# Kernel tuning notes

Hardware: AMD Instinct MI355X
Metric: run time of the kernel (lower is better)

The kernel has to match this reference:

```python
import jax, jax.numpy as jnp
import numpy as np

K_F = 3
NUM = K_F * K_F - 1      # 8 non-reference neighbors
IDX_REF = NUM // 2       # 4: reference pixel inserted in the middle
PROP_TIME = 18


def _conv2d(x, w, b, pad):
    y = jax.lax.conv_general_dilated(x, w, (1, 1), [(pad, pad), (pad, pad)],
                                     dimension_numbers=("NCHW", "OIHW", "NCHW"))
    return y + b[None, :, None, None]


def _offset_affinity(guidance, conv_w, conv_b, aff_scale):
    # TGASS branch of _get_offset_affinity
    B, _, H, W = guidance.shape
    pad_g = (conv_w.shape[2] - 1) // 2
    oa = _conv2d(guidance, conv_w, conv_b, pad_g)          # [B, 3*NUM, H, W]
    o1, o2, aff = jnp.split(oa, 3, axis=1)
    # torch: cat((o1,o2),1).view(B, NUM, 2, H, W) -- plain reinterpret of channels
    off = jnp.concatenate([o1, o2], axis=1).reshape(B, NUM, 2, H, W)
    zeros = jnp.zeros((B, 1, 2, H, W), off.dtype)
    off = jnp.concatenate([off[:, :IDX_REF], zeros, off[:, IDX_REF:]], axis=1)  # [B,9,2,H,W]
    aff = jnp.tanh(aff) / (aff_scale + 1e-8)               # TGASS scaling
    s = jnp.sum(jnp.abs(aff), axis=1, keepdims=True) + 1e-4
    s = jnp.maximum(s, 1.0)                                # aff_abs_sum[<1]=1
    aff = aff / s
    aff_ref = 1.0 - jnp.sum(aff, axis=1, keepdims=True)
    aff = jnp.concatenate([aff[:, :IDX_REF], aff_ref, aff[:, IDX_REF:]], axis=1)  # [B,9,H,W]
    return off.reshape(B, 2 * (NUM + 1), H, W), aff


def _bilinear(img, y, x):
    # img [B,H,W]; y,x [B,K,H,W] absolute sampling coords; zero outside (DCN zero padding)
    H, W = img.shape[1], img.shape[2]
    y0 = jnp.floor(y)
    x0 = jnp.floor(x)
    ty = y - y0
    tx = x - x0

    def g(yi, xi):
        valid = (yi >= 0) & (yi <= H - 1) & (xi >= 0) & (xi <= W - 1)
        yc = jnp.clip(yi, 0, H - 1).astype(jnp.int32)
        xc = jnp.clip(xi, 0, W - 1).astype(jnp.int32)
        v = jax.vmap(lambda im, a, b: im[a, b])(img, yc, xc)
        return jnp.where(valid, v, 0.0)

    return ((1 - ty) * (1 - tx) * g(y0, x0) + (1 - ty) * tx * g(y0, x0 + 1)
            + ty * (1 - tx) * g(y0 + 1, x0) + ty * tx * g(y0 + 1, x0 + 1))


def _nlspn_forward(feat_init, guidance, confidence, conv_w, conv_b, aff_scale):
    B, _, H, W = feat_init.shape
    dt = feat_init.dtype
    offset, aff = _offset_affinity(guidance, conv_w, conv_b, aff_scale)
    off = offset.reshape(B, NUM + 1, 2, H, W)
    off_y, off_x = off[:, :, 0], off[:, :, 1]              # [B,9,H,W]
    kk = jnp.arange(NUM + 1)
    grid_y = (kk // K_F - 1).astype(dt)[None, :, None, None]
    grid_x = (kk % K_F - 1).astype(dt)[None, :, None, None]
    base_y = jnp.arange(H, dtype=dt)[None, None, :, None]
    base_x = jnp.arange(W, dtype=dt)[None, None, None, :]
    # absolute sampling coordinates, constant across propagation steps
    yy = base_y + grid_y + off_y                           # [B,9,H,W]
    xx = base_x + grid_x + off_x

    def step(feat, _):
        # modulated deform conv with w==1, b==0, groups=1: weighted gather-sum
        s = _bilinear((feat * confidence)[:, 0], yy, xx)   # [B,9,H,W]
        nf = jnp.sum(aff * s, axis=1, keepdims=True)       # [B,1,H,W]
        return nf, nf

    feat_final, feats = jax.lax.scan(step, feat_init, None, length=PROP_TIME)
    return feat_final, feats, offset, aff, aff_scale


def setup_inputs() -> dict:
    key = jax.random.key(0)
    k1, k2, k3, k4 = jax.random.split(key, 4)
    B, CG, H, W = 4, 8, 240, 1216
    feat_init = jax.random.uniform(k1, (B, 1, H, W), dtype=jnp.float32)
    guidance = jax.random.normal(k2, (B, CG, H, W), dtype=jnp.float32)
    confidence = jax.random.uniform(k3, (B, 1, H, W), dtype=jnp.float32)
    conv_w = 0.1 * jax.random.normal(k4, (3 * NUM, CG, 3, 3), dtype=jnp.float32)
    conv_b = jnp.zeros((3 * NUM,), jnp.float32)
    aff_scale = jnp.full((1,), 0.5 * NUM, jnp.float32)     # affinity_gamma * num
    return {"feat_init": feat_init, "guidance": guidance, "confidence": confidence,
            "conv_w": conv_w, "conv_b": conv_b, "aff_scale": aff_scale}


def reference(feat_init, guidance, confidence, conv_w, conv_b, aff_scale):
    return _nlspn_forward(feat_init, guidance, confidence, conv_w, conv_b, aff_scale)
```

## Files before the change

kernel.cpp:

```cpp
#include <hip/hip_runtime.h>

#define BB 4
#define CG 8
#define HH 240
#define WW 1216
#define HW (HH*WW)
#define NPIX (BB*HW)

#define TW 128
#define TH 4
#define MG 8
#define LW (TW + 2*MG)
#define LH (TH + 2*MG)
#define NXT ((WW + TW - 1)/TW)
#define NYT (HH/TH)

#define CBX 19
#define CBY 60

struct TapR { unsigned pack, frac; float av; };

__global__ __launch_bounds__(256) void conv_fused(
    const float* __restrict__ g, const float* __restrict__ cw,
    const float* __restrict__ cb, const float* __restrict__ asc,
    const float* __restrict__ feat_init, const float* __restrict__ conf,
    float* __restrict__ out_off, float* __restrict__ out_aff,
    float* __restrict__ out_scale,
    TapR* __restrict__ tpr, float* __restrict__ fc0)
{
    int bx = blockIdx.x % CBX;
    int by = blockIdx.x / CBX;
    int b  = blockIdx.y;
    if (blockIdx.x == 0 && b == 0 && threadIdx.x == 0) out_scale[0] = asc[0];

    int tx = threadIdx.x & 63;
    int ty = threadIdx.x >> 6;
    int w = bx * 64 + tx;
    int h = by * 4 + ty;
    int pix = h * WW + w;
    int gid = b * HW + pix;

    const float* gb = g + (size_t)b * CG * HW;

    float gvals[9 * CG];
    bool interior = (bx > 0) & (bx < CBX - 1) & (by > 0) & (by < CBY - 1);
    if (interior) {
        const float* p = gb + (h - 1) * WW + (w - 1);
        #pragma unroll
        for (int ch = 0; ch < CG; ++ch)
            #pragma unroll
            for (int kh = 0; kh < 3; ++kh)
                #pragma unroll
                for (int kw = 0; kw < 3; ++kw)
                    gvals[ch * 9 + kh * 3 + kw] = p[(size_t)ch * HW + kh * WW + kw];
    } else {
        #pragma unroll
        for (int kh = 0; kh < 3; ++kh) {
            int y = h + kh - 1;
            float my = ((unsigned)y < (unsigned)HH) ? 1.0f : 0.0f;
            int yc = min(max(y, 0), HH - 1);
            #pragma unroll
            for (int kw = 0; kw < 3; ++kw) {
                int x = w + kw - 1;
                float m = ((unsigned)x < (unsigned)WW) ? my : 0.0f;
                int xc = min(max(x, 0), WW - 1);
                const float* p = gb + yc * WW + xc;
                #pragma unroll
                for (int ch = 0; ch < CG; ++ch)
                    gvals[ch * 9 + kh * 3 + kw] = m * p[(size_t)ch * HW];
            }
        }
    }

    float acc[24];
    #pragma unroll
    for (int o = 0; o < 24; ++o) acc[o] = cb[o];

    #pragma unroll
    for (int ch = 0; ch < CG; ++ch) {
        #pragma unroll
        for (int kh = 0; kh < 3; ++kh) {
            #pragma unroll
            for (int kw = 0; kw < 3; ++kw) {
                float xv = gvals[ch * 9 + kh * 3 + kw];
                #pragma unroll
                for (int o = 0; o < 24; ++o)
                    acc[o] = fmaf(xv, cw[((o * CG + ch) * 3 + kh) * 3 + kw], acc[o]);
            }
        }
    }

    float oyk[9], oxk[9];
    #pragma unroll
    for (int k = 0; k < 9; ++k) {
        if (k < 4)       { oyk[k] = acc[2 * k];     oxk[k] = acc[2 * k + 1]; }
        else if (k == 4) { oyk[k] = 0.0f;           oxk[k] = 0.0f; }
        else             { oyk[k] = acc[2 * k - 2]; oxk[k] = acc[2 * k - 1]; }
        __builtin_nontemporal_store(oyk[k], &out_off[(size_t)(b * 18 + 2 * k) * HW + pix]);
        __builtin_nontemporal_store(oxk[k], &out_off[(size_t)(b * 18 + 2 * k + 1) * HW + pix]);
    }

    float inv = 1.0f / (asc[0] + 1e-8f);
    float a[8];
    float s = 0.0f;
    #pragma unroll
    for (int c = 0; c < 8; ++c) {
        a[c] = tanhf(acc[16 + c]) * inv;
        s += fabsf(a[c]);
    }
    s += 1e-4f;
    s = fmaxf(s, 1.0f);
    float sum = 0.0f;
    #pragma unroll
    for (int c = 0; c < 8; ++c) {
        a[c] = a[c] / s;
        sum += a[c];
    }
    float a9[9];
    #pragma unroll
    for (int c = 0; c < 4; ++c) a9[c] = a[c];
    a9[4] = 1.0f - sum;
    #pragma unroll
    for (int c = 4; c < 8; ++c) a9[c + 1] = a[c];

    #pragma unroll
    for (int k = 0; k < 9; ++k)
        __builtin_nontemporal_store(a9[k], &out_aff[(size_t)(b * 9 + k) * HW + pix]);

    if (tpr) {
        #pragma unroll
        for (int k = 0; k < 9; ++k) {
            if (k == 4) continue;
            int j = (k < 4) ? k : k - 1;

            float yy = (float)(h + k / 3 - 1) + oyk[k];
            float xx = (float)(w + k % 3 - 1) + oxk[k];
            float y0f = floorf(yy), x0f = floorf(xx);
            float tyf = yy - y0f, txf = xx - x0f;

            unsigned vy0 = (y0f >= 0.0f   && y0f <= 239.0f)  ? 1u : 0u;
            unsigned vy1 = (y0f >= -1.0f  && y0f <= 238.0f)  ? 1u : 0u;
            unsigned vx0 = (x0f >= 0.0f   && x0f <= 1215.0f) ? 1u : 0u;
            unsigned vx1 = (x0f >= -1.0f  && x0f <= 1214.0f) ? 1u : 0u;

            int y0i = (int)fminf(fmaxf(y0f, -1.0f), 239.0f);
            int x0i = (int)fminf(fmaxf(x0f, -1.0f), 1215.0f);

            unsigned pack = (unsigned)(y0i + 1) | ((unsigned)(x0i + 1) << 8)
                          | (vy0 << 19) | (vy1 << 20) | (vx0 << 21) | (vx1 << 22);
            unsigned tyq = (unsigned)(fminf(tyf, 0.99999f) * 65535.0f + 0.5f);
            unsigned txq = (unsigned)(fminf(txf, 0.99999f) * 65535.0f + 0.5f);

            TapR r;
            r.pack = pack;
            r.frac = tyq | (txq << 16);
            r.av   = a9[k];
            tpr[(size_t)j * NPIX + gid] = r;
        }
        fc0[gid] = feat_init[gid] * conf[gid];
    }
}

__global__ __launch_bounds__(512) void prop4(
    const float* __restrict__ fcIn, const float* __restrict__ conf,
    const TapR* __restrict__ tpr, const float* __restrict__ affq,
    float* __restrict__ fout, float* __restrict__ fcOut, float* __restrict__ ffinal)
{
    __shared__ float sfc[LH * LW];

    int bx = blockIdx.x % NXT;
    int by = blockIdx.x / NXT;
    int b  = blockIdx.y;
    int xs = bx * TW, ys = by * TH;

    int rlo = max(0, ys - MG), rhi = min(HH - 1, ys + TH - 1 + MG);
    int clo = max(0, xs - MG), chi = min(WW - 1, xs + TW - 1 + MG);
    int rh = rhi - rlo + 1;

    const float* fcb = fcIn + (size_t)b * HW;

    for (int i = threadIdx.x; i < rh * LW; i += 512) {
        int r = i / LW;
        int c = i - r * LW;
        int col = min(clo + c, WW - 1);
        sfc[i] = fcb[(rlo + r) * WW + col];
    }
    __syncthreads();

    int tx = threadIdx.x & (TW - 1);
    int tyy = threadIdx.x >> 7;
    int x = xs + tx, y = ys + tyy;
    if (x >= WW) return;
    int pix = y * WW + x;
    int gid = b * HW + pix;

    float res = affq[(size_t)(b * 9 + 4) * HW + pix] *
                sfc[(y - rlo) * LW + (x - clo)];

    #pragma unroll
    for (int j = 0; j < 8; ++j) {
        TapR t = tpr[(size_t)j * NPIX + gid];
        unsigned Px = t.pack;
        unsigned Py = t.frac;
        float    av = t.av;

        int y0 = (int)(Px & 0xffu) - 1;
        int x0 = (int)((Px >> 8) & 0x7ffu) - 1;
        float ty = (float)(Py & 0xffffu) * (1.0f / 65535.0f);
        float txf = (float)(Py >> 16)    * (1.0f / 65535.0f);
        float fy0 = (Px & (1u << 19)) ? 1.0f : 0.0f;
        float fy1 = (Px & (1u << 20)) ? 1.0f : 0.0f;
        float fx0 = (Px & (1u << 21)) ? 1.0f : 0.0f;
        float fx1 = (Px & (1u << 22)) ? 1.0f : 0.0f;

        int yA = max(y0, 0), yB = min(y0 + 1, HH - 1);
        int xA = max(x0, 0), xB = min(x0 + 1, WW - 1);

        float v00, v01, v10, v11;
        if (yA >= rlo && yB <= rhi && xA >= clo && xB <= chi) {
            int rA = (yA - rlo) * LW - clo;
            int rB = (yB - rlo) * LW - clo;
            v00 = sfc[rA + xA]; v01 = sfc[rA + xB];
            v10 = sfc[rB + xA]; v11 = sfc[rB + xB];
        } else {
            int rA = yA * WW, rB = yB * WW;
            v00 = fcb[rA + xA]; v01 = fcb[rA + xB];
            v10 = fcb[rB + xA]; v11 = fcb[rB + xB];
        }

        float cy0 = fy0 * (1.0f - ty),  cy1 = fy1 * ty;
        float cx0 = fx0 * (1.0f - txf), cx1 = fx1 * txf;

        float u0 = fmaf(cx1, v01, cx0 * v00);
        float u1 = fmaf(cx1, v11, cx0 * v10);
        res = fmaf(av, fmaf(cy1, u1, cy0 * u0), res);
    }
    __builtin_nontemporal_store(res, &fout[gid]);
    if (fcOut)  fcOut[gid] = res * conf[gid];
    if (ffinal) __builtin_nontemporal_store(res, &ffinal[gid]);
}

__device__ __forceinline__ float sampPC(const float* __restrict__ fb,
                                        const float* __restrict__ cf,
                                        int y, int x) {
    bool valid = ((unsigned)y < (unsigned)HH) && ((unsigned)x < (unsigned)WW);
    int yc = min(max(y, 0), HH - 1);
    int xc = min(max(x, 0), WW - 1);
    int idx = yc * WW + xc;
    float v = fb[idx] * cf[idx];
    return valid ? v : 0.0f;
}

__global__ __launch_bounds__(256) void prop(
    const float* __restrict__ fp, const float* __restrict__ conf,
    const float* __restrict__ off, const float* __restrict__ aff,
    float* __restrict__ fout, float* __restrict__ ffinal)
{
    int gid = blockIdx.x * 256 + threadIdx.x;
    if (gid >= NPIX) return;
    int w = gid % WW;
    int tmp = gid / WW;
    int h = tmp % HH;
    int b = tmp / HH;
    int pix = h * WW + w;

    const float* fb = fp + (size_t)b * HW;
    const float* cf = conf + (size_t)b * HW;

    float res = 0.0f;
    #pragma unroll
    for (int k = 0; k < 9; ++k) {
        float oy = off[(size_t)(b * 18 + 2 * k) * HW + pix];
        float ox = off[(size_t)(b * 18 + 2 * k + 1) * HW + pix];
        float av = aff[(size_t)(b * 9 + k) * HW + pix];

        float yy = (float)(h + k / 3 - 1) + oy;
        float xx = (float)(w + k % 3 - 1) + ox;

        float y0f = floorf(yy), x0f = floorf(xx);
        float ty = yy - y0f, tx = xx - x0f;
        int y0 = (int)y0f, x0 = (int)x0f;

        float v00 = sampPC(fb, cf, y0,     x0);
        float v01 = sampPC(fb, cf, y0,     x0 + 1);
        float v10 = sampPC(fb, cf, y0 + 1, x0);
        float v11 = sampPC(fb, cf, y0 + 1, x0 + 1);

        float sk = (1.0f - ty) * (1.0f - tx) * v00
                 + (1.0f - ty) * tx          * v01
                 + ty          * (1.0f - tx) * v10
                 + ty          * tx          * v11;
        res = fmaf(av, sk, res);
    }
    fout[gid] = res;
    if (ffinal) ffinal[gid] = res;
}

extern "C" void kernel_launch(void* const* d_in, const int* in_sizes, int n_in,
                              void* d_out, int out_size, void* d_ws, size_t ws_size,
                              hipStream_t stream) {
    const float* feat_init  = (const float*)d_in[0];
    const float* guidance   = (const float*)d_in[1];
    const float* confidence = (const float*)d_in[2];
    const float* conv_w     = (const float*)d_in[3];
    const float* conv_b     = (const float*)d_in[4];
    const float* aff_scale  = (const float*)d_in[5];

    float* out        = (float*)d_out;
    float* feat_final = out;
    float* feats      = out + (size_t)NPIX;
    float* offset     = out + (size_t)19 * NPIX;
    float* affout     = out + (size_t)37 * NPIX;
    float* scale_out  = out + (size_t)46 * NPIX;

    size_t need = (size_t)8 * NPIX * 12 + (size_t)2 * NPIX * 4;

    dim3 cgrid(CBX * CBY, BB);

    if (ws_size >= need) {
        char* wsb = (char*)d_ws;
        TapR*  tpr = (TapR*)wsb;
        float* fcA = (float*)(wsb + (size_t)8 * NPIX * 12);
        float* fcB = fcA + NPIX;

        conv_fused<<<cgrid, 256, 0, stream>>>(guidance, conv_w, conv_b, aff_scale,
                                              feat_init, confidence,
                                              offset, affout, scale_out,
                                              tpr, fcA);

        dim3 pgrid(NXT * NYT, BB);
        float* fcIn = fcA;
        float* fcOut = fcB;
        for (int t = 0; t < 18; ++t) {
            float* cur = feats + (size_t)t * NPIX;
            prop4<<<pgrid, 512, 0, stream>>>(fcIn, confidence, tpr, affout, cur,
                                             (t == 17) ? nullptr : fcOut,
                                             (t == 17) ? feat_final : nullptr);
            float* tmpp = fcIn; fcIn = fcOut; fcOut = tmpp;
        }
    } else {
        conv_fused<<<cgrid, 256, 0, stream>>>(guidance, conv_w, conv_b, aff_scale,
                                              feat_init, confidence,
                                              offset, affout, scale_out,
                                              nullptr, nullptr);
        const float* prev = feat_init;
        int nblocks = (NPIX + 255) / 256;
        for (int t = 0; t < 18; ++t) {
            float* cur = feats + (size_t)t * NPIX;
            prop<<<nblocks, 256, 0, stream>>>(prev, confidence, offset, affout, cur,
                                              (t == 17) ? feat_final : nullptr);
            prev = cur;
        }
    }
}
```

Baseline: 633.2 us.

## Transpose conv weights for packed FMA and fold confidence multiply into propagation tile load

```diff
diff --git a/kernel.cpp b/kernel.cpp
--- a/kernel.cpp
+++ b/kernel.cpp
@@ -18,15 +18,26 @@
 #define CBX 19
 #define CBY 60
 
+typedef float f32x2 __attribute__((ext_vector_type(2)));
+
 struct TapR { unsigned pack, frac; float av; };
 
+__global__ __launch_bounds__(256) void transpose_w(
+    const float* __restrict__ cw, float* __restrict__ wt)
+{
+    int i = blockIdx.x * 256 + threadIdx.x;
+    if (i >= 24 * 72) return;
+    int o = i % 24;
+    int r = i / 24;
+    wt[r * 24 + o] = cw[o * 72 + r];
+}
+
 __global__ __launch_bounds__(256) void conv_fused(
-    const float* __restrict__ g, const float* __restrict__ cw,
+    const float* __restrict__ g, const float* __restrict__ wt,
     const float* __restrict__ cb, const float* __restrict__ asc,
-    const float* __restrict__ feat_init, const float* __restrict__ conf,
     float* __restrict__ out_off, float* __restrict__ out_aff,
     float* __restrict__ out_scale,
-    TapR* __restrict__ tpr, float* __restrict__ fc0)
+    TapR* __restrict__ tpr)
 {
     int bx = blockIdx.x % CBX;
     int by = blockIdx.x / CBX;
@@ -40,19 +51,19 @@
     int pix = h * WW + w;
     int gid = b * HW + pix;
 
-    const float* gb = g + (size_t)b * CG * HW;
+    const float* gb = g + b * (CG * HW);
 
     float gvals[9 * CG];
     bool interior = (bx > 0) & (bx < CBX - 1) & (by > 0) & (by < CBY - 1);
     if (interior) {
-        const float* p = gb + (h - 1) * WW + (w - 1);
+        int base = (h - 1) * WW + (w - 1);
         #pragma unroll
         for (int ch = 0; ch < CG; ++ch)
             #pragma unroll
             for (int kh = 0; kh < 3; ++kh)
                 #pragma unroll
                 for (int kw = 0; kw < 3; ++kw)
-                    gvals[ch * 9 + kh * 3 + kw] = p[(size_t)ch * HW + kh * WW + kw];
+                    gvals[ch * 9 + kh * 3 + kw] = gb[base + ch * HW + kh * WW + kw];
     } else {
         #pragma unroll
         for (int kh = 0; kh < 3; ++kh) {
@@ -64,17 +75,18 @@
                 int x = w + kw - 1;
                 float m = ((unsigned)x < (unsigned)WW) ? my : 0.0f;
                 int xc = min(max(x, 0), WW - 1);
-                const float* p = gb + yc * WW + xc;
+                int base = yc * WW + xc;
                 #pragma unroll
                 for (int ch = 0; ch < CG; ++ch)
-                    gvals[ch * 9 + kh * 3 + kw] = m * p[(size_t)ch * HW];
+                    gvals[ch * 9 + kh * 3 + kw] = m * gb[base + ch * HW];
             }
         }
     }
 
-    float acc[24];
-    #pragma unroll
-    for (int o = 0; o < 24; ++o) acc[o] = cb[o];
+    f32x2 acc2[12];
+    const f32x2* cb2 = (const f32x2*)cb;
+    #pragma unroll
+    for (int o2 = 0; o2 < 12; ++o2) acc2[o2] = cb2[o2];
 
     #pragma unroll
     for (int ch = 0; ch < CG; ++ch) {
@@ -83,12 +95,18 @@
             #pragma unroll
             for (int kw = 0; kw < 3; ++kw) {
                 float xv = gvals[ch * 9 + kh * 3 + kw];
+                f32x2 xv2; xv2[0] = xv; xv2[1] = xv;
+                const f32x2* wp = (const f32x2*)(wt + (ch * 9 + kh * 3 + kw) * 24);
                 #pragma unroll
-                for (int o = 0; o < 24; ++o)
-                    acc[o] = fmaf(xv, cw[((o * CG + ch) * 3 + kh) * 3 + kw], acc[o]);
+                for (int o2 = 0; o2 < 12; ++o2)
+                    acc2[o2] = __builtin_elementwise_fma(xv2, wp[o2], acc2[o2]);
             }
         }
     }
+
+    float acc[24];
+    #pragma unroll
+    for (int o = 0; o < 24; ++o) acc[o] = acc2[o >> 1][o & 1];
 
     float oyk[9], oxk[9];
     #pragma unroll
@@ -157,14 +175,13 @@
             r.av   = a9[k];
             tpr[(size_t)j * NPIX + gid] = r;
         }
-        fc0[gid] = feat_init[gid] * conf[gid];
-    }
-}
-
-__global__ __launch_bounds__(512) void prop4(
-    const float* __restrict__ fcIn, const float* __restrict__ conf,
+    }
+}
+
+__global__ __launch_bounds__(512) void prop5(
+    const float* __restrict__ fprev, const float* __restrict__ conf,
     const TapR* __restrict__ tpr, const float* __restrict__ affq,
-    float* __restrict__ fout, float* __restrict__ fcOut, float* __restrict__ ffinal)
+    float* __restrict__ fout, float* __restrict__ ffinal)
 {
     __shared__ float sfc[LH * LW];
 
@@ -177,13 +194,15 @@
     int clo = max(0, xs - MG), chi = min(WW - 1, xs + TW - 1 + MG);
     int rh = rhi - rlo + 1;
 
-    const float* fcb = fcIn + (size_t)b * HW;
+    const float* fpb = fprev + b * HW;
+    const float* cfb = conf + b * HW;
 
     for (int i = threadIdx.x; i < rh * LW; i += 512) {
         int r = i / LW;
         int c = i - r * LW;
         int col = min(clo + c, WW - 1);
-        sfc[i] = fcb[(rlo + r) * WW + col];
+        int idx = (rlo + r) * WW + col;
+        sfc[i] = fpb[idx] * cfb[idx];
     }
     __syncthreads();
 
@@ -224,8 +243,10 @@
             v10 = sfc[rB + xA]; v11 = sfc[rB + xB];
         } else {
             int rA = yA * WW, rB = yB * WW;
-            v00 = fcb[rA + xA]; v01 = fcb[rA + xB];
-            v10 = fcb[rB + xA]; v11 = fcb[rB + xB];
+            v00 = fpb[rA + xA] * cfb[rA + xA];
+            v01 = fpb[rA + xB] * cfb[rA + xB];
+            v10 = fpb[rB + xA] * cfb[rB + xA];
+            v11 = fpb[rB + xB] * cfb[rB + xB];
         }
 
         float cy0 = fy0 * (1.0f - ty),  cy1 = fy1 * ty;
@@ -235,8 +256,7 @@
         float u1 = fmaf(cx1, v11, cx0 * v10);
         res = fmaf(av, fmaf(cy1, u1, cy0 * u0), res);
     }
-    __builtin_nontemporal_store(res, &fout[gid]);
-    if (fcOut)  fcOut[gid] = res * conf[gid];
+    fout[gid] = res;
     if (ffinal) __builtin_nontemporal_store(res, &ffinal[gid]);
 }
 
@@ -313,36 +333,33 @@
     float* affout     = out + (size_t)37 * NPIX;
     float* scale_out  = out + (size_t)46 * NPIX;
 
-    size_t need = (size_t)8 * NPIX * 12 + (size_t)2 * NPIX * 4;
+    size_t tpr_bytes = (size_t)8 * NPIX * 12;
+    size_t need = tpr_bytes + 1728 * 4;
 
     dim3 cgrid(CBX * CBY, BB);
 
     if (ws_size >= need) {
         char* wsb = (char*)d_ws;
         TapR*  tpr = (TapR*)wsb;
-        float* fcA = (float*)(wsb + (size_t)8 * NPIX * 12);
-        float* fcB = fcA + NPIX;
-
-        conv_fused<<<cgrid, 256, 0, stream>>>(guidance, conv_w, conv_b, aff_scale,
-                                              feat_init, confidence,
-                                              offset, affout, scale_out,
-                                              tpr, fcA);
+        float* wt  = (float*)(wsb + tpr_bytes);
+
+        transpose_w<<<7, 256, 0, stream>>>(conv_w, wt);
+        conv_fused<<<cgrid, 256, 0, stream>>>(guidance, wt, conv_b, aff_scale,
+                                              offset, affout, scale_out, tpr);
 
         dim3 pgrid(NXT * NYT, BB);
-        float* fcIn = fcA;
-        float* fcOut = fcB;
+        const float* prev = feat_init;
         for (int t = 0; t < 18; ++t) {
             float* cur = feats + (size_t)t * NPIX;
-            prop4<<<pgrid, 512, 0, stream>>>(fcIn, confidence, tpr, affout, cur,
-                                             (t == 17) ? nullptr : fcOut,
+            prop5<<<pgrid, 512, 0, stream>>>(prev, confidence, tpr, affout, cur,
                                              (t == 17) ? feat_final : nullptr);
-            float* tmpp = fcIn; fcIn = fcOut; fcOut = tmpp;
-        }
-    } else {
-        conv_fused<<<cgrid, 256, 0, stream>>>(guidance, conv_w, conv_b, aff_scale,
-                                              feat_init, confidence,
-                                              offset, affout, scale_out,
-                                              nullptr, nullptr);
+            prev = cur;
+        }
+    } else if (ws_size >= 1728 * 4) {
+        float* wt = (float*)d_ws;
+        transpose_w<<<7, 256, 0, stream>>>(conv_w, wt);
+        conv_fused<<<cgrid, 256, 0, stream>>>(guidance, wt, conv_b, aff_scale,
+                                              offset, affout, scale_out, nullptr);
         const float* prev = feat_init;
         int nblocks = (NPIX + 255) / 256;
         for (int t = 0; t < 18; ++t) {
```

Measured after the change: 819.7 us. 1.29x slower.
